# Kernel optimization log

Measured on AMD Instinct MI355X. Metric: run time of the kernel, lower is better.

The kernel has to match this reference:

```python
import jax, jax.numpy as jnp
import numpy as np

B, F0, D = 512, 40, 32
SIZES = [200, 200, 200]


def _glorot(key, shape):
    fan_in, fan_out = shape[0], shape[1]
    std = np.sqrt(2.0 / (fan_in + fan_out)).astype(np.float32)
    return jax.random.normal(key, shape, dtype=jnp.float32) * std


def setup_inputs() -> dict:
    key = jax.random.key(0)
    k0, k1, k2, k3 = jax.random.split(key, 4)
    inputs = jax.random.normal(k0, (B, F0, D), dtype=jnp.float32)
    # weights: (field_i * field_0, next_size), matching tf conv1d filter (1, Fi*F0, next)
    W0 = _glorot(k1, (F0 * F0, SIZES[0]))
    W1 = _glorot(k2, (SIZES[0] * F0, SIZES[1]))
    W2 = _glorot(k3, (SIZES[1] * F0, SIZES[2]))
    return {"inputs": inputs, "W0": W0, "W1": W1, "W2": W2}


def _cin(inputs, Ws):
    # inputs: [B, F0, D]; each layer: outer product along field dims per embedding dim,
    # then a 1x1 'conv' (GEMM) mixing the F0*Fi interaction axis down to next size.
    h = inputs
    outs = []
    for W in Ws:
        # z[b,i,j,d] = x0[b,i,d] * h[b,j,d]  -> flatten (i,j) row-major (matches tf reshape)
        z = jnp.einsum('bid,bjd->bijd', inputs, h)
        b, f0, fi, d = z.shape
        z = z.reshape(b, f0 * fi, d)
        # conv1d with kernel width 1 == GEMM over the interaction axis
        h = jnp.einsum('bkd,kn->bnd', z, W)  # [B, next, D]
        outs.append(h)
    out = jnp.concatenate(outs, axis=1)      # [B, sum(sizes), D]
    return jnp.sum(out, axis=-1)             # [B, sum(sizes)]


def reference(inputs, W0, W1, W2):
    return _cin(inputs, [W0, W1, W2])
```

## Files before the change

kernel.cpp:

```cpp
#include <hip/hip_runtime.h>

#define CIN_B 512
#define CIN_F0 40
#define CIN_D 32
#define CIN_S 200

typedef _Float16 f16x8 __attribute__((ext_vector_type(8)));
typedef _Float16 f16x2 __attribute__((ext_vector_type(2)));
typedef float floatx16 __attribute__((ext_vector_type(16)));

__device__ __forceinline__ unsigned short f2h(float f) {
    _Float16 h = (_Float16)f;
    return *(unsigned short*)&h;
}
__device__ __forceinline__ float h2f(unsigned short u) {
    return (float)(*(_Float16*)&u);
}
__device__ __forceinline__ f16x8 mulbc(f16x8 v, unsigned int s2) {
    union { unsigned int u; f16x2 p; } sc; sc.u = s2;
    union { f16x8 h; f16x2 p[4]; } a, r;
    a.h = v;
#pragma unroll
    for (int q = 0; q < 4; ++q) r.p[q] = a.p[q] * sc.p;
    return r.h;
}

__global__ __launch_bounds__(256) void prep_all(
    const float* __restrict__ X,  const float* __restrict__ W0,
    const float* __restrict__ W1, const float* __restrict__ W2,
    unsigned short* __restrict__ Wtk1, unsigned short* __restrict__ Wtk2,
    unsigned short* __restrict__ W2t,  unsigned short* __restrict__ X0hd,
    unsigned short* __restrict__ Xh) {
    __shared__ unsigned short T[32][33];
    const int bid = blockIdx.x;

    if (bid < 120) {
        const int kc = bid, nn = threadIdx.x;
        const int i = kc / 3, kk = kc - i * 3;
        unsigned short v[16];
#pragma unroll
        for (int kw = 0; kw < 16; ++kw) {
            int j = kk * 16 + kw;
            float f = 0.f;
            if (j < CIN_F0 && nn < CIN_S) f = W0[(size_t)(i * CIN_F0 + j) * CIN_S + nn];
            v[kw] = f2h(f);
        }
        uint4* dst = (uint4*)(Wtk1 + ((size_t)kc * 256 + nn) * 16);
        dst[0] = ((const uint4*)v)[0];
        dst[1] = ((const uint4*)v)[1];
    } else if (bid < 640) {
        const int kc = bid - 120, nn = threadIdx.x;
        const int i = kc / 13, kk = kc - i * 13;
        const float sc = (kk == 6) ? 0.5f : 1.0f;
        unsigned short v[16];
#pragma unroll
        for (int kw = 0; kw < 16; ++kw) {
            int j = kk * 16 + kw;
            float f = 0.f;
            if (j < CIN_S && nn < CIN_S) f = sc * W1[(size_t)(i * CIN_S + j) * CIN_S + nn];
            v[kw] = f2h(f);
        }
        uint4* dst = (uint4*)(Wtk2 + ((size_t)kc * 256 + nn) * 16);
        dst[0] = ((const uint4*)v)[0];
        dst[1] = ((const uint4*)v)[1];
    } else if (bid < 2432) {
        const int q0 = bid - 640;
        const int kt = q0 & 255, nt = q0 >> 8;
        const int tx = threadIdx.x & 31, ty = threadIdx.x >> 5;
#pragma unroll
        for (int q = 0; q < 4; ++q) {
            int kl = ty + 8 * q;
            int k = kt * 32 + kl, n = nt * 32 + tx;
            float f = (k < 8000 && n < CIN_S) ? W2[(size_t)k * CIN_S + n] : 0.f;
            T[kl][tx] = f2h(f);
        }
        __syncthreads();
#pragma unroll
        for (int q = 0; q < 4; ++q) {
            int nl = ty + 8 * q;
            W2t[(size_t)(nt * 32 + nl) * 8192 + kt * 32 + tx] = T[tx][nl];
        }
    } else {
        int e = (bid - 2432) * 256 + threadIdx.x;
        int d = e & 31;
        int rest = e >> 5;
        int i = rest % CIN_F0;
        int b = rest / CIN_F0;
        unsigned short v = f2h(X[e]);
        Xh[e] = v;
        X0hd[((size_t)b * CIN_D + d) * 48 + i] = v;
        if (e < CIN_B * CIN_D * 8) {
            int q = e & 7, dd = (e >> 3) & 31, bb = e >> 8;
            X0hd[((size_t)bb * CIN_D + dd) * 48 + 40 + q] = 0;
        }
    }
}

template <int NKC, int KCPI_TOT, int JROW, int MODE, int NB, int WPS>
__global__ __launch_bounds__(448, WPS)
void cin_layer(const unsigned short* __restrict__ Hsrc,
               const unsigned short* __restrict__ Xh,
               const unsigned short* __restrict__ Wtk,
               unsigned short* __restrict__ Hout,
               float* __restrict__ outp) {
    __shared__ __align__(16) unsigned short Bp[NB * NKC * 512];
    __shared__ unsigned int Xl[CIN_F0 * CIN_D];

    const int tid = threadIdx.x;
    const int b0 = blockIdx.x * NB;
    const int jh = (MODE == 1) ? 0 : blockIdx.y;
    const int kks = jh * 6;

    for (int e = tid; e < CIN_F0 * CIN_D; e += 448) {
        unsigned int lo = Xh[(size_t)b0 * (CIN_F0 * CIN_D) + e];
        unsigned int hi = (NB == 2) ? (unsigned int)Xh[(size_t)(b0 + 1) * (CIN_F0 * CIN_D) + e] : 0u;
        Xl[e] = lo | (hi << 16);
    }
    {
        const int j0 = (MODE == 1) ? 0 : jh * 96;
        uint4* Bpu = (uint4*)Bp;
        for (int g = tid; g < NB * 64 * NKC; g += 448) {
            int bb = g / (64 * NKC), r = g - bb * (64 * NKC);
            int d = r / (2 * NKC), c = r - d * (2 * NKC);
            uint4 v = ((const uint4*)Hsrc)[(((size_t)(b0 + bb) * CIN_D + d) * JROW + j0) / 8 + c];
            Bpu[(bb * NKC + (c >> 1)) * 64 + (c & 1) * 32 + d] = v;
        }
    }
    __syncthreads();

    const int wave = tid >> 6, lane = tid & 63;
    const int l32 = lane & 31, hl = lane >> 5;
    const int tile = wave;

    const int aB = (tile * 32 + l32) * 16 + hl * 8;
    constexpr int NS = 20 * NKC;

    f16x8 Ar[2][2];
    f16x8 Br[2][NB];

    auto ldA = [&](int s, int slot) {
        int ss = (s < NS) ? s : (NS - 1);
        int iA = 2 * (ss / NKC), kk = ss % NKC;
        int e = (iA * KCPI_TOT + kks + kk) * 4096 + aB;
        Ar[slot][0] = *(const f16x8*)(Wtk + e);
        Ar[slot][1] = *(const f16x8*)(Wtk + e + KCPI_TOT * 4096);
    };
    auto ldB = [&](int s, int slot) {
        int ss = (s < NS) ? s : (NS - 1);
        int kk = ss % NKC;
        Br[slot][0] = *(const f16x8*)&Bp[(0 * NKC + kk) * 512 + lane * 8];
        if constexpr (NB == 2)
            Br[slot][1] = *(const f16x8*)&Bp[(1 * NKC + kk) * 512 + lane * 8];
    };

    ldA(0, 0);
    ldA(1, 1);
    ldB(0, 0);

    floatx16 acc0, acc1;
#pragma unroll
    for (int r = 0; r < 16; ++r) acc0[r] = 0.f;
    if constexpr (NB == 2) {
#pragma unroll
        for (int r = 0; r < 16; ++r) acc1[r] = 0.f;
    }
    unsigned int xs0a = 0, xs1a = 0, xs0b = 0, xs1b = 0;

#pragma unroll 1
    for (int s0 = 0; s0 < NS; s0 += 2 * NKC) {
#pragma unroll
        for (int t = 0; t < 2 * NKC; ++t) {
            const int s = s0 + t;
            const int kk = t % NKC;
            if (kk == 0) {
                const int iA = (s0 / NKC + (t ? 1 : 0)) * 2;
                unsigned int xpa = Xl[iA * CIN_D + l32];
                unsigned int xpb = Xl[(iA + 1) * CIN_D + l32];
                xs0a = (xpa & 0xffffu) | (xpa << 16);
                xs0b = (xpb & 0xffffu) | (xpb << 16);
                if constexpr (NB == 2) {
                    xs1a = (xpa >> 16) | (xpa & 0xffff0000u);
                    xs1b = (xpb >> 16) | (xpb & 0xffff0000u);
                }
            }
            ldB(s + 1, (t + 1) & 1);
            const int sl = t & 1;
            acc0 = __builtin_amdgcn_mfma_f32_32x32x16_f16(
                Ar[sl][0], mulbc(Br[sl][0], xs0a), acc0, 0, 0, 0);
            if constexpr (NB == 2)
                acc1 = __builtin_amdgcn_mfma_f32_32x32x16_f16(
                    Ar[sl][0], mulbc(Br[sl][1], xs1a), acc1, 0, 0, 0);
            acc0 = __builtin_amdgcn_mfma_f32_32x32x16_f16(
                Ar[sl][1], mulbc(Br[sl][0], xs0b), acc0, 0, 0, 0);
            if constexpr (NB == 2)
                acc1 = __builtin_amdgcn_mfma_f32_32x32x16_f16(
                    Ar[sl][1], mulbc(Br[sl][1], xs1b), acc1, 0, 0, 0);
            ldA(s + 2, sl);
        }
    }

#pragma unroll
    for (int bb = 0; bb < NB; ++bb) {
        const floatx16& a = bb ? acc1 : acc0;

        if constexpr (MODE == 1) {
            unsigned short* dst =
                Hout + ((size_t)(b0 + bb) * CIN_D + l32) * 224 + tile * 32;
#pragma unroll
            for (int qd = 0; qd < 4; ++qd) {
                ushort4 pk;
                pk.x = f2h(a[4 * qd + 0]);
                pk.y = f2h(a[4 * qd + 1]);
                pk.z = f2h(a[4 * qd + 2]);
                pk.w = f2h(a[4 * qd + 3]);
                *(ushort4*)&dst[8 * qd + 4 * hl] = pk;
            }
        }
        if constexpr (MODE == 2) {
            unsigned short* hb2 =
                Hout + (((size_t)jh * CIN_B + b0 + bb) * 208) * CIN_D + l32;
#pragma unroll
            for (int r = 0; r < 16; ++r) {
                int n = tile * 32 + (r & 3) + 8 * (r >> 2) + 4 * hl;
                if (n < 208) hb2[(size_t)n * CIN_D] = f2h(a[r]);
            }
        }

#pragma unroll
        for (int r = 0; r < 16; ++r) {
            float v = a[r];
            v += __shfl_xor(v, 1);
            v += __shfl_xor(v, 2);
            v += __shfl_xor(v, 4);
            v += __shfl_xor(v, 8);
            v += __shfl_xor(v, 16);
            if (l32 == 0) {
                int n = tile * 32 + (r & 3) + 8 * (r >> 2) + 4 * hl;
                if (n < CIN_S) {
                    if constexpr (MODE == 1)
                        outp[(size_t)(b0 + bb) * 600 + n] = v;
                    else
                        outp[((size_t)jh * CIN_B + b0 + bb) * CIN_S + n] = v;
                }
            }
        }
    }
}

__global__ __launch_bounds__(448) void cin_g(const unsigned short* __restrict__ Xh,
                                             const unsigned short* __restrict__ Hacc,
                                             unsigned short* __restrict__ G) {
    const int b = blockIdx.x;
    const int wave = threadIdx.x >> 6, lane = threadIdx.x & 63;
    const int l32 = lane & 31, hl = lane >> 5;
    const int jt = wave;

    if (wave == 0 && lane < 24) {
        uint4 z; z.x = z.y = z.z = z.w = 0;
        ((uint4*)(G + (size_t)b * 8192 + 8000))[lane] = z;
    }

    f16x8 zed;
#pragma unroll
    for (int q = 0; q < 8; ++q) zed[q] = (_Float16)0.f;

    f16x8 a[2][2];
#pragma unroll
    for (int it = 0; it < 2; ++it) {
        int i = it * 32 + l32;
#pragma unroll
        for (int kh = 0; kh < 2; ++kh)
            a[it][kh] = (i < CIN_F0)
                ? *(const f16x8*)&Xh[((size_t)b * CIN_F0 + i) * CIN_D + kh * 16 + hl * 8]
                : zed;
    }

    const int j = jt * 32 + l32;
    const unsigned short* p0 = Hacc + ((size_t)b * 208 + j) * CIN_D;
    const unsigned short* p1 = Hacc + ((size_t)(CIN_B + b) * 208 + j) * CIN_D;
    f16x8 bf[2];
#pragma unroll
    for (int kh = 0; kh < 2; ++kh)
        bf[kh] = (j < 208)
            ? (*(const f16x8*)(p0 + kh * 16 + hl * 8) +
               *(const f16x8*)(p1 + kh * 16 + hl * 8))
            : zed;

#pragma unroll
    for (int it = 0; it < 2; ++it) {
        floatx16 acc;
#pragma unroll
        for (int r = 0; r < 16; ++r) acc[r] = 0.f;
        acc = __builtin_amdgcn_mfma_f32_32x32x16_f16(a[it][0], bf[0], acc, 0, 0, 0);
        acc = __builtin_amdgcn_mfma_f32_32x32x16_f16(a[it][1], bf[1], acc, 0, 0, 0);
#pragma unroll
        for (int r = 0; r < 16; ++r) {
            int row = (r & 3) + 8 * (r >> 2) + 4 * hl;
            int i = it * 32 + row, jj = jt * 32 + l32;
            if (i < CIN_F0 && jj < CIN_S)
                G[(size_t)b * 8192 + i * CIN_S + jj] = f2h(acc[r]);
        }
    }
}

__global__ __launch_bounds__(64) void cin_l3(const unsigned short* __restrict__ W2t,
                                             const unsigned short* __restrict__ G,
                                             float* __restrict__ outp3) {
    const int mt = blockIdx.x;
    const int bt = blockIdx.y;
    const int kch = blockIdx.z;
    const int lane = threadIdx.x, l32 = lane & 31, hl = lane >> 5;

    const unsigned short* pa = W2t + (size_t)(mt * 32 + l32) * 8192 + kch * 512 + hl * 8;
    const unsigned short* pb = G   + (size_t)(bt * 32 + l32) * 8192 + kch * 512 + hl * 8;

    floatx16 acc;
#pragma unroll
    for (int r = 0; r < 16; ++r) acc[r] = 0.f;

    f16x8 Aa[2], Bb[2];
    Aa[0] = *(const f16x8*)(pa);       Bb[0] = *(const f16x8*)(pb);
    Aa[1] = *(const f16x8*)(pa + 16);  Bb[1] = *(const f16x8*)(pb + 16);

#pragma unroll 1
    for (int s0 = 0; s0 < 32; s0 += 2) {
#pragma unroll
        for (int t = 0; t < 2; ++t) {
            acc = __builtin_amdgcn_mfma_f32_32x32x16_f16(Aa[t], Bb[t], acc, 0, 0, 0);
            Aa[t] = *(const f16x8*)(pa + (s0 + t + 2) * 16);
            Bb[t] = *(const f16x8*)(pb + (s0 + t + 2) * 16);
        }
    }

#pragma unroll
    for (int r = 0; r < 16; ++r) {
        int n = mt * 32 + (r & 3) + 8 * (r >> 2) + 4 * hl;
        if (n < CIN_S)
            outp3[((size_t)kch * CIN_B + bt * 32 + l32) * CIN_S + n] = acc[r];
    }
}

__global__ __launch_bounds__(256) void cin_outc(const float* __restrict__ p2,
                                                const float* __restrict__ p3,
                                                float* __restrict__ out) {
    int e = blockIdx.x * 256 + threadIdx.x;
    int b = e / 400, t = e - b * 400;
    int half = t / 200, n = t - half * 200;
    float s;
    if (half == 0) {
        s = p2[(size_t)b * CIN_S + n] + p2[(size_t)(CIN_B + b) * CIN_S + n];
    } else {
        s = 0.f;
#pragma unroll
        for (int q = 0; q < 16; ++q)
            s += p3[((size_t)q * CIN_B + b) * CIN_S + n];
    }
    out[(size_t)b * 600 + 200 + half * 200 + n] = s;
}

extern "C" void kernel_launch(void* const* d_in, const int* in_sizes, int n_in,
                              void* d_out, int out_size, void* d_ws, size_t ws_size,
                              hipStream_t stream) {
    const float* X  = (const float*)d_in[0];
    const float* W0 = (const float*)d_in[1];
    const float* W1 = (const float*)d_in[2];
    const float* W2 = (const float*)d_in[3];
    float* out = (float*)d_out;

    unsigned short* Wtk1 = (unsigned short*)d_ws;
    unsigned short* Wtk2 = Wtk1 + (size_t)120 * 4096;
    unsigned short* W2t  = Wtk2 + (size_t)520 * 4096;
    unsigned short* X0hd = W2t + (size_t)224 * 8192;
    unsigned short* Xh   = X0hd + (size_t)CIN_B * CIN_D * 48;
    unsigned short* H1   = Xh + (size_t)CIN_B * CIN_F0 * CIN_D;
    unsigned short* Hacc = H1 + (size_t)CIN_B * CIN_D * 224;
    float* outp2 = (float*)(Hacc + (size_t)2 * CIN_B * 208 * CIN_D);
    float* outp3 = outp2 + (size_t)2 * CIN_B * CIN_S;
    unsigned short* G = (unsigned short*)(outp3 + (size_t)16 * CIN_B * CIN_S);

    prep_all<<<4992, 256, 0, stream>>>(X, W0, W1, W2, Wtk1, Wtk2, W2t, X0hd, Xh);

    cin_layer<3, 3, 48, 1, 2, 4><<<dim3(CIN_B / 2, 1), 448, 0, stream>>>(
        X0hd, Xh, Wtk1, H1, out);
    cin_layer<7, 13, 224, 2, 2, 4><<<dim3(CIN_B / 2, 2), 448, 0, stream>>>(
        H1, Xh, Wtk2, Hacc, outp2);

    cin_g<<<CIN_B, 448, 0, stream>>>(Xh, Hacc, G);
    cin_l3<<<dim3(7, 16, 16), 64, 0, stream>>>(W2t, G, outp3);

    cin_outc<<<(CIN_B * 400) / 256, 256, 0, stream>>>(outp2, outp3, out);
}
```

Measured before the change: 209.5 us.

## Split layer-1 interaction axis across two blocks with partial-sum reduction

Layer 1 now runs over a 2D grid that splits the i (field) reduction into two halves. Each half writes a partial fp16 H1 buffer and partial row sums. Layer 2 adds the two partial H1 buffers when it loads its B tiles, and the final combine kernel also reduces the layer-1 partial sums. The aim is to double the block count of the small first layer for better occupancy and latency hiding. The cost is extra partial-buffer traffic, an fp16 rounding of the partials before summation, and G now aliasing the H1 buffer.

```diff
diff --git a/kernel.cpp b/kernel.cpp
--- a/kernel.cpp
+++ b/kernel.cpp
@@ -96,33 +96,42 @@
     }
 }
 
-template <int NKC, int KCPI_TOT, int JROW, int MODE, int NB, int WPS>
-__global__ __launch_bounds__(448, WPS)
+template <int NKC, int KCPI_TOT, int JROW, int MODE, int IH, bool HSUM>
+__global__ __launch_bounds__(448, 4)
 void cin_layer(const unsigned short* __restrict__ Hsrc,
                const unsigned short* __restrict__ Xh,
                const unsigned short* __restrict__ Wtk,
                unsigned short* __restrict__ Hout,
                float* __restrict__ outp) {
-    __shared__ __align__(16) unsigned short Bp[NB * NKC * 512];
+    __shared__ __align__(16) unsigned short Bp[2 * NKC * 512];
     __shared__ unsigned int Xl[CIN_F0 * CIN_D];
 
     const int tid = threadIdx.x;
-    const int b0 = blockIdx.x * NB;
+    const int b0 = blockIdx.x * 2;
     const int jh = (MODE == 1) ? 0 : blockIdx.y;
+    const int ih = (MODE == 1 && IH == 2) ? blockIdx.y : 0;
     const int kks = jh * 6;
+    constexpr int IBASE_STEP = CIN_F0 / IH;
 
     for (int e = tid; e < CIN_F0 * CIN_D; e += 448) {
         unsigned int lo = Xh[(size_t)b0 * (CIN_F0 * CIN_D) + e];
-        unsigned int hi = (NB == 2) ? (unsigned int)Xh[(size_t)(b0 + 1) * (CIN_F0 * CIN_D) + e] : 0u;
+        unsigned int hi = Xh[(size_t)(b0 + 1) * (CIN_F0 * CIN_D) + e];
         Xl[e] = lo | (hi << 16);
     }
     {
         const int j0 = (MODE == 1) ? 0 : jh * 96;
+        constexpr size_t HPART = (size_t)CIN_B * CIN_D * 224;
         uint4* Bpu = (uint4*)Bp;
-        for (int g = tid; g < NB * 64 * NKC; g += 448) {
+        for (int g = tid; g < 2 * 64 * NKC; g += 448) {
             int bb = g / (64 * NKC), r = g - bb * (64 * NKC);
             int d = r / (2 * NKC), c = r - d * (2 * NKC);
-            uint4 v = ((const uint4*)Hsrc)[(((size_t)(b0 + bb) * CIN_D + d) * JROW + j0) / 8 + c];
+            size_t idx = (((size_t)(b0 + bb) * CIN_D + d) * JROW + j0) / 8 + c;
+            uint4 v = ((const uint4*)Hsrc)[idx];
+            if constexpr (HSUM) {
+                uint4 v1 = ((const uint4*)(Hsrc + HPART))[idx];
+                f16x8 s = *(f16x8*)&v + *(f16x8*)&v1;
+                v = *(uint4*)&s;
+            }
             Bpu[(bb * NKC + (c >> 1)) * 64 + (c & 1) * 32 + d] = v;
         }
     }
@@ -134,23 +143,27 @@
 
     const int aB = (tile * 32 + l32) * 16 + hl * 8;
     constexpr int NS = 20 * NKC;
+    constexpr int NSI = NS / IH;
+
+    const unsigned short* WtkB =
+        Wtk + (size_t)(ih * IBASE_STEP) * KCPI_TOT * 4096;
+    const unsigned int* XlB = Xl + ih * IBASE_STEP * CIN_D;
 
     f16x8 Ar[2][2];
-    f16x8 Br[2][NB];
+    f16x8 Br[2][2];
 
     auto ldA = [&](int s, int slot) {
-        int ss = (s < NS) ? s : (NS - 1);
+        int ss = (s < NSI) ? s : (NSI - 1);
         int iA = 2 * (ss / NKC), kk = ss % NKC;
-        int e = (iA * KCPI_TOT + kks + kk) * 4096 + aB;
-        Ar[slot][0] = *(const f16x8*)(Wtk + e);
-        Ar[slot][1] = *(const f16x8*)(Wtk + e + KCPI_TOT * 4096);
+        size_t e = (size_t)(iA * KCPI_TOT + kks + kk) * 4096 + aB;
+        Ar[slot][0] = *(const f16x8*)(WtkB + e);
+        Ar[slot][1] = *(const f16x8*)(WtkB + e + (size_t)KCPI_TOT * 4096);
     };
     auto ldB = [&](int s, int slot) {
-        int ss = (s < NS) ? s : (NS - 1);
+        int ss = (s < NSI) ? s : (NSI - 1);
         int kk = ss % NKC;
         Br[slot][0] = *(const f16x8*)&Bp[(0 * NKC + kk) * 512 + lane * 8];
-        if constexpr (NB == 2)
-            Br[slot][1] = *(const f16x8*)&Bp[(1 * NKC + kk) * 512 + lane * 8];
+        Br[slot][1] = *(const f16x8*)&Bp[(1 * NKC + kk) * 512 + lane * 8];
     };
 
     ldA(0, 0);
@@ -159,53 +172,46 @@
 
     floatx16 acc0, acc1;
 #pragma unroll
-    for (int r = 0; r < 16; ++r) acc0[r] = 0.f;
-    if constexpr (NB == 2) {
-#pragma unroll
-        for (int r = 0; r < 16; ++r) acc1[r] = 0.f;
-    }
+    for (int r = 0; r < 16; ++r) { acc0[r] = 0.f; acc1[r] = 0.f; }
     unsigned int xs0a = 0, xs1a = 0, xs0b = 0, xs1b = 0;
 
 #pragma unroll 1
-    for (int s0 = 0; s0 < NS; s0 += 2 * NKC) {
+    for (int s0 = 0; s0 < NSI; s0 += 2 * NKC) {
 #pragma unroll
         for (int t = 0; t < 2 * NKC; ++t) {
             const int s = s0 + t;
             const int kk = t % NKC;
             if (kk == 0) {
                 const int iA = (s0 / NKC + (t ? 1 : 0)) * 2;
-                unsigned int xpa = Xl[iA * CIN_D + l32];
-                unsigned int xpb = Xl[(iA + 1) * CIN_D + l32];
+                unsigned int xpa = XlB[iA * CIN_D + l32];
+                unsigned int xpb = XlB[(iA + 1) * CIN_D + l32];
                 xs0a = (xpa & 0xffffu) | (xpa << 16);
+                xs1a = (xpa >> 16) | (xpa & 0xffff0000u);
                 xs0b = (xpb & 0xffffu) | (xpb << 16);
-                if constexpr (NB == 2) {
-                    xs1a = (xpa >> 16) | (xpa & 0xffff0000u);
-                    xs1b = (xpb >> 16) | (xpb & 0xffff0000u);
-                }
+                xs1b = (xpb >> 16) | (xpb & 0xffff0000u);
             }
             ldB(s + 1, (t + 1) & 1);
             const int sl = t & 1;
             acc0 = __builtin_amdgcn_mfma_f32_32x32x16_f16(
                 Ar[sl][0], mulbc(Br[sl][0], xs0a), acc0, 0, 0, 0);
-            if constexpr (NB == 2)
-                acc1 = __builtin_amdgcn_mfma_f32_32x32x16_f16(
-                    Ar[sl][0], mulbc(Br[sl][1], xs1a), acc1, 0, 0, 0);
+            acc1 = __builtin_amdgcn_mfma_f32_32x32x16_f16(
+                Ar[sl][0], mulbc(Br[sl][1], xs1a), acc1, 0, 0, 0);
             acc0 = __builtin_amdgcn_mfma_f32_32x32x16_f16(
                 Ar[sl][1], mulbc(Br[sl][0], xs0b), acc0, 0, 0, 0);
-            if constexpr (NB == 2)
-                acc1 = __builtin_amdgcn_mfma_f32_32x32x16_f16(
-                    Ar[sl][1], mulbc(Br[sl][1], xs1b), acc1, 0, 0, 0);
+            acc1 = __builtin_amdgcn_mfma_f32_32x32x16_f16(
+                Ar[sl][1], mulbc(Br[sl][1], xs1b), acc1, 0, 0, 0);
             ldA(s + 2, sl);
         }
     }
 
 #pragma unroll
-    for (int bb = 0; bb < NB; ++bb) {
+    for (int bb = 0; bb < 2; ++bb) {
         const floatx16& a = bb ? acc1 : acc0;
 
         if constexpr (MODE == 1) {
             unsigned short* dst =
-                Hout + ((size_t)(b0 + bb) * CIN_D + l32) * 224 + tile * 32;
+                Hout + (size_t)ih * CIN_B * CIN_D * 224 +
+                ((size_t)(b0 + bb) * CIN_D + l32) * 224 + tile * 32;
 #pragma unroll
             for (int qd = 0; qd < 4; ++qd) {
                 ushort4 pk;
@@ -226,6 +232,7 @@
             }
         }
 
+        const int part = (MODE == 1) ? ih : jh;
 #pragma unroll
         for (int r = 0; r < 16; ++r) {
             float v = a[r];
@@ -236,12 +243,8 @@
             v += __shfl_xor(v, 16);
             if (l32 == 0) {
                 int n = tile * 32 + (r & 3) + 8 * (r >> 2) + 4 * hl;
-                if (n < CIN_S) {
-                    if constexpr (MODE == 1)
-                        outp[(size_t)(b0 + bb) * 600 + n] = v;
-                    else
-                        outp[((size_t)jh * CIN_B + b0 + bb) * CIN_S + n] = v;
-                }
+                if (n < CIN_S)
+                    outp[((size_t)part * CIN_B + b0 + bb) * CIN_S + n] = v;
             }
         }
     }
@@ -340,14 +343,17 @@
     }
 }
 
-__global__ __launch_bounds__(256) void cin_outc(const float* __restrict__ p2,
+__global__ __launch_bounds__(256) void cin_outc(const float* __restrict__ p1,
+                                                const float* __restrict__ p2,
                                                 const float* __restrict__ p3,
                                                 float* __restrict__ out) {
     int e = blockIdx.x * 256 + threadIdx.x;
-    int b = e / 400, t = e - b * 400;
-    int half = t / 200, n = t - half * 200;
+    int b = e / 600, t = e - b * 600;
+    int sec = t / 200, n = t - sec * 200;
     float s;
-    if (half == 0) {
+    if (sec == 0) {
+        s = p1[(size_t)b * CIN_S + n] + p1[(size_t)(CIN_B + b) * CIN_S + n];
+    } else if (sec == 1) {
         s = p2[(size_t)b * CIN_S + n] + p2[(size_t)(CIN_B + b) * CIN_S + n];
     } else {
         s = 0.f;
@@ -355,7 +361,7 @@
         for (int q = 0; q < 16; ++q)
             s += p3[((size_t)q * CIN_B + b) * CIN_S + n];
     }
-    out[(size_t)b * 600 + 200 + half * 200 + n] = s;
+    out[e] = s;
 }
 
 extern "C" void kernel_launch(void* const* d_in, const int* in_sizes, int n_in,
@@ -372,21 +378,22 @@
     unsigned short* W2t  = Wtk2 + (size_t)520 * 4096;
     unsigned short* X0hd = W2t + (size_t)224 * 8192;
     unsigned short* Xh   = X0hd + (size_t)CIN_B * CIN_D * 48;
-    unsigned short* H1   = Xh + (size_t)CIN_B * CIN_F0 * CIN_D;
-    unsigned short* Hacc = H1 + (size_t)CIN_B * CIN_D * 224;
-    float* outp2 = (float*)(Hacc + (size_t)2 * CIN_B * 208 * CIN_D);
+    unsigned short* H1p  = Xh + (size_t)CIN_B * CIN_F0 * CIN_D;
+    unsigned short* Hacc = H1p + (size_t)2 * CIN_B * CIN_D * 224;
+    float* outp1 = (float*)(Hacc + (size_t)2 * CIN_B * 208 * CIN_D);
+    float* outp2 = outp1 + (size_t)2 * CIN_B * CIN_S;
     float* outp3 = outp2 + (size_t)2 * CIN_B * CIN_S;
-    unsigned short* G = (unsigned short*)(outp3 + (size_t)16 * CIN_B * CIN_S);
+    unsigned short* G = H1p;
 
     prep_all<<<4992, 256, 0, stream>>>(X, W0, W1, W2, Wtk1, Wtk2, W2t, X0hd, Xh);
 
-    cin_layer<3, 3, 48, 1, 2, 4><<<dim3(CIN_B / 2, 1), 448, 0, stream>>>(
-        X0hd, Xh, Wtk1, H1, out);
-    cin_layer<7, 13, 224, 2, 2, 4><<<dim3(CIN_B / 2, 2), 448, 0, stream>>>(
-        H1, Xh, Wtk2, Hacc, outp2);
+    cin_layer<3, 3, 48, 1, 2, false><<<dim3(CIN_B / 2, 2), 448, 0, stream>>>(
+        X0hd, Xh, Wtk1, H1p, outp1);
+    cin_layer<7, 13, 224, 2, 1, true><<<dim3(CIN_B / 2, 2), 448, 0, stream>>>(
+        H1p, Xh, Wtk2, Hacc, outp2);
 
     cin_g<<<CIN_B, 448, 0, stream>>>(Xh, Hacc, G);
     cin_l3<<<dim3(7, 16, 16), 64, 0, stream>>>(W2t, G, outp3);
 
-    cin_outc<<<(CIN_B * 400) / 256, 256, 0, stream>>>(outp2, outp3, out);
-}
+    cin_outc<<<(CIN_B * 600) / 256, 256, 0, stream>>>(outp1, outp2, outp3, out);
+}
```

Result: no change. 212.6 us (+1.5%).

## Stage layer-2 weights through an LDS ring via async global-to-LDS loads

Applied to the files above, without the earlier changes.

Layer 2 now runs as a 896-thread block covering four batch rows. The block's two wave groups share weight tiles that are streamed into a 4-slot LDS ring with global_load_lds, paced by vmcnt waits and barriers. Before, each wave loaded A fragments straight from global memory per step. The goal is to cut redundant global weight traffic and overlap weight fetches with MFMA work, at the cost of a barrier per step and larger LDS use, which may lower occupancy. Layer 1 is split into its own specialised kernel.

```diff
diff --git a/kernel.cpp b/kernel.cpp
--- a/kernel.cpp
+++ b/kernel.cpp
@@ -23,6 +23,11 @@
 #pragma unroll
     for (int q = 0; q < 4; ++q) r.p[q] = a.p[q] * sc.p;
     return r.h;
+}
+__device__ __forceinline__ void gload_lds16(const unsigned short* g, unsigned short* l) {
+    __builtin_amdgcn_global_load_lds(
+        (const __attribute__((address_space(1))) void*)(const void*)g,
+        (__attribute__((address_space(3))) void*)(void*)l, 16, 0, 0);
 }
 
 __global__ __launch_bounds__(256) void prep_all(
@@ -96,33 +101,30 @@
     }
 }
 
-template <int NKC, int KCPI_TOT, int JROW, int MODE, int NB, int WPS>
-__global__ __launch_bounds__(448, WPS)
-void cin_layer(const unsigned short* __restrict__ Hsrc,
-               const unsigned short* __restrict__ Xh,
-               const unsigned short* __restrict__ Wtk,
-               unsigned short* __restrict__ Hout,
-               float* __restrict__ outp) {
-    __shared__ __align__(16) unsigned short Bp[NB * NKC * 512];
+template <int NKC, int KCPI_TOT, int JROW>
+__global__ __launch_bounds__(448, 4)
+void cin_layer1(const unsigned short* __restrict__ Hsrc,
+                const unsigned short* __restrict__ Xh,
+                const unsigned short* __restrict__ Wtk,
+                unsigned short* __restrict__ Hout,
+                float* __restrict__ outp) {
+    __shared__ __align__(16) unsigned short Bp[2 * NKC * 512];
     __shared__ unsigned int Xl[CIN_F0 * CIN_D];
 
     const int tid = threadIdx.x;
-    const int b0 = blockIdx.x * NB;
-    const int jh = (MODE == 1) ? 0 : blockIdx.y;
-    const int kks = jh * 6;
+    const int b0 = blockIdx.x * 2;
 
     for (int e = tid; e < CIN_F0 * CIN_D; e += 448) {
         unsigned int lo = Xh[(size_t)b0 * (CIN_F0 * CIN_D) + e];
-        unsigned int hi = (NB == 2) ? (unsigned int)Xh[(size_t)(b0 + 1) * (CIN_F0 * CIN_D) + e] : 0u;
+        unsigned int hi = Xh[(size_t)(b0 + 1) * (CIN_F0 * CIN_D) + e];
         Xl[e] = lo | (hi << 16);
     }
     {
-        const int j0 = (MODE == 1) ? 0 : jh * 96;
         uint4* Bpu = (uint4*)Bp;
-        for (int g = tid; g < NB * 64 * NKC; g += 448) {
+        for (int g = tid; g < 2 * 64 * NKC; g += 448) {
             int bb = g / (64 * NKC), r = g - bb * (64 * NKC);
             int d = r / (2 * NKC), c = r - d * (2 * NKC);
-            uint4 v = ((const uint4*)Hsrc)[(((size_t)(b0 + bb) * CIN_D + d) * JROW + j0) / 8 + c];
+            uint4 v = ((const uint4*)Hsrc)[(((size_t)(b0 + bb) * CIN_D + d) * JROW) / 8 + c];
             Bpu[(bb * NKC + (c >> 1)) * 64 + (c & 1) * 32 + d] = v;
         }
     }
@@ -136,12 +138,12 @@
     constexpr int NS = 20 * NKC;
 
     f16x8 Ar[2][2];
-    f16x8 Br[2][NB];
+    f16x8 Br[2][2];
 
     auto ldA = [&](int s, int slot) {
         int ss = (s < NS) ? s : (NS - 1);
         int iA = 2 * (ss / NKC), kk = ss % NKC;
-        int e = (iA * KCPI_TOT + kks + kk) * 4096 + aB;
+        int e = (iA * KCPI_TOT + kk) * 4096 + aB;
         Ar[slot][0] = *(const f16x8*)(Wtk + e);
         Ar[slot][1] = *(const f16x8*)(Wtk + e + KCPI_TOT * 4096);
     };
@@ -149,8 +151,7 @@
         int ss = (s < NS) ? s : (NS - 1);
         int kk = ss % NKC;
         Br[slot][0] = *(const f16x8*)&Bp[(0 * NKC + kk) * 512 + lane * 8];
-        if constexpr (NB == 2)
-            Br[slot][1] = *(const f16x8*)&Bp[(1 * NKC + kk) * 512 + lane * 8];
+        Br[slot][1] = *(const f16x8*)&Bp[(1 * NKC + kk) * 512 + lane * 8];
     };
 
     ldA(0, 0);
@@ -159,11 +160,7 @@
 
     floatx16 acc0, acc1;
 #pragma unroll
-    for (int r = 0; r < 16; ++r) acc0[r] = 0.f;
-    if constexpr (NB == 2) {
-#pragma unroll
-        for (int r = 0; r < 16; ++r) acc1[r] = 0.f;
-    }
+    for (int r = 0; r < 16; ++r) { acc0[r] = 0.f; acc1[r] = 0.f; }
     unsigned int xs0a = 0, xs1a = 0, xs0b = 0, xs1b = 0;
 
 #pragma unroll 1
@@ -177,55 +174,38 @@
                 unsigned int xpa = Xl[iA * CIN_D + l32];
                 unsigned int xpb = Xl[(iA + 1) * CIN_D + l32];
                 xs0a = (xpa & 0xffffu) | (xpa << 16);
+                xs1a = (xpa >> 16) | (xpa & 0xffff0000u);
                 xs0b = (xpb & 0xffffu) | (xpb << 16);
-                if constexpr (NB == 2) {
-                    xs1a = (xpa >> 16) | (xpa & 0xffff0000u);
-                    xs1b = (xpb >> 16) | (xpb & 0xffff0000u);
-                }
+                xs1b = (xpb >> 16) | (xpb & 0xffff0000u);
             }
             ldB(s + 1, (t + 1) & 1);
             const int sl = t & 1;
             acc0 = __builtin_amdgcn_mfma_f32_32x32x16_f16(
                 Ar[sl][0], mulbc(Br[sl][0], xs0a), acc0, 0, 0, 0);
-            if constexpr (NB == 2)
-                acc1 = __builtin_amdgcn_mfma_f32_32x32x16_f16(
-                    Ar[sl][0], mulbc(Br[sl][1], xs1a), acc1, 0, 0, 0);
+            acc1 = __builtin_amdgcn_mfma_f32_32x32x16_f16(
+                Ar[sl][0], mulbc(Br[sl][1], xs1a), acc1, 0, 0, 0);
             acc0 = __builtin_amdgcn_mfma_f32_32x32x16_f16(
                 Ar[sl][1], mulbc(Br[sl][0], xs0b), acc0, 0, 0, 0);
-            if constexpr (NB == 2)
-                acc1 = __builtin_amdgcn_mfma_f32_32x32x16_f16(
-                    Ar[sl][1], mulbc(Br[sl][1], xs1b), acc1, 0, 0, 0);
+            acc1 = __builtin_amdgcn_mfma_f32_32x32x16_f16(
+                Ar[sl][1], mulbc(Br[sl][1], xs1b), acc1, 0, 0, 0);
             ldA(s + 2, sl);
         }
     }
 
 #pragma unroll
-    for (int bb = 0; bb < NB; ++bb) {
+    for (int bb = 0; bb < 2; ++bb) {
         const floatx16& a = bb ? acc1 : acc0;
-
-        if constexpr (MODE == 1) {
-            unsigned short* dst =
-                Hout + ((size_t)(b0 + bb) * CIN_D + l32) * 224 + tile * 32;
-#pragma unroll
-            for (int qd = 0; qd < 4; ++qd) {
-                ushort4 pk;
-                pk.x = f2h(a[4 * qd + 0]);
-                pk.y = f2h(a[4 * qd + 1]);
-                pk.z = f2h(a[4 * qd + 2]);
-                pk.w = f2h(a[4 * qd + 3]);
-                *(ushort4*)&dst[8 * qd + 4 * hl] = pk;
-            }
-        }
-        if constexpr (MODE == 2) {
-            unsigned short* hb2 =
-                Hout + (((size_t)jh * CIN_B + b0 + bb) * 208) * CIN_D + l32;
-#pragma unroll
-            for (int r = 0; r < 16; ++r) {
-                int n = tile * 32 + (r & 3) + 8 * (r >> 2) + 4 * hl;
-                if (n < 208) hb2[(size_t)n * CIN_D] = f2h(a[r]);
-            }
-        }
-
+        unsigned short* dst =
+            Hout + ((size_t)(b0 + bb) * CIN_D + l32) * 224 + tile * 32;
+#pragma unroll
+        for (int qd = 0; qd < 4; ++qd) {
+            ushort4 pk;
+            pk.x = f2h(a[4 * qd + 0]);
+            pk.y = f2h(a[4 * qd + 1]);
+            pk.z = f2h(a[4 * qd + 2]);
+            pk.w = f2h(a[4 * qd + 3]);
+            *(ushort4*)&dst[8 * qd + 4 * hl] = pk;
+        }
 #pragma unroll
         for (int r = 0; r < 16; ++r) {
             float v = a[r];
@@ -236,12 +216,133 @@
             v += __shfl_xor(v, 16);
             if (l32 == 0) {
                 int n = tile * 32 + (r & 3) + 8 * (r >> 2) + 4 * hl;
-                if (n < CIN_S) {
-                    if constexpr (MODE == 1)
-                        outp[(size_t)(b0 + bb) * 600 + n] = v;
-                    else
-                        outp[((size_t)jh * CIN_B + b0 + bb) * CIN_S + n] = v;
-                }
+                if (n < CIN_S) outp[(size_t)(b0 + bb) * 600 + n] = v;
+            }
+        }
+    }
+}
+
+template <int NKC, int KCPI_TOT, int JROW>
+__global__ __launch_bounds__(896, 4)
+void cin_l2s(const unsigned short* __restrict__ Hsrc,
+             const unsigned short* __restrict__ Xh,
+             const unsigned short* __restrict__ Wtk,
+             unsigned short* __restrict__ Hout,
+             float* __restrict__ outp) {
+    __shared__ __align__(16) unsigned short Bp[4 * NKC * 512];
+    __shared__ unsigned int Xl[2][CIN_F0 * CIN_D];
+    __shared__ __align__(16) unsigned short Ring[4 * 7 * 512 * 2];
+
+    const int tid = threadIdx.x;
+    const int b0 = blockIdx.x * 4;
+    const int jh = blockIdx.y;
+    const int kks = jh * 6;
+    constexpr int NS = 20 * NKC;
+
+    for (int e = tid; e < 2 * CIN_F0 * CIN_D; e += 896) {
+        int pair = e / (CIN_F0 * CIN_D), ee = e - pair * (CIN_F0 * CIN_D);
+        unsigned int lo = Xh[(size_t)(b0 + 2 * pair) * (CIN_F0 * CIN_D) + ee];
+        unsigned int hi = Xh[(size_t)(b0 + 2 * pair + 1) * (CIN_F0 * CIN_D) + ee];
+        Xl[pair][ee] = lo | (hi << 16);
+    }
+    {
+        const int j0 = jh * 96;
+        uint4* Bpu = (uint4*)Bp;
+        for (int g = tid; g < 4 * 64 * NKC; g += 896) {
+            int bb = g / (64 * NKC), r = g - bb * (64 * NKC);
+            int d = r / (2 * NKC), c = r - d * (2 * NKC);
+            uint4 v = ((const uint4*)Hsrc)[(((size_t)(b0 + bb) * CIN_D + d) * JROW + j0) / 8 + c];
+            Bpu[(bb * NKC + (c >> 1)) * 64 + (c & 1) * 32 + d] = v;
+        }
+    }
+
+    const int wave = tid >> 6, lane = tid & 63;
+    const int l32 = lane & 31, hl = lane >> 5;
+    const int wg = wave / 7;
+    const int nt = wave - wg * 7;
+    constexpr int SLOT = 7 * 512 * 2;
+
+    const unsigned short* gS =
+        Wtk + (size_t)(kks + wg * KCPI_TOT) * 4096 + (size_t)(nt * 64 + lane) * 8;
+    const int destB = wg * 3584 + nt * 512;
+
+#pragma unroll
+    for (int s = 0; s < 3; ++s) {
+        gload_lds16(gS, Ring + s * SLOT + destB);
+        gS += 4096;
+    }
+    __syncthreads();
+
+    const unsigned short* BpW = Bp + (size_t)(2 * wg) * NKC * 512 + lane * 8;
+    const unsigned short* ringR = Ring + l32 * 16 + hl * 8 + nt * 512;
+    const unsigned int* XlW = Xl[wg] + l32;
+
+    floatx16 acc0, acc1;
+#pragma unroll
+    for (int r = 0; r < 16; ++r) { acc0[r] = 0.f; acc1[r] = 0.f; }
+    unsigned int xs0a = 0, xs1a = 0, xs0b = 0, xs1b = 0;
+
+#pragma unroll 1
+    for (int s0 = 0; s0 < NS; s0 += 2 * NKC) {
+#pragma unroll
+        for (int t = 0; t < 2 * NKC; ++t) {
+            const int kk = t % NKC;
+            asm volatile("s_waitcnt vmcnt(2)" ::: "memory");
+            asm volatile("s_barrier" ::: "memory");
+            gload_lds16(gS, Ring + ((s0 + t + 3) & 3) * SLOT + destB);
+            {
+                const int kk3 = (t + 3) % NKC;
+                gS += (kk3 == NKC - 1) ? (size_t)(2 * KCPI_TOT - (NKC - 1)) * 4096
+                                       : (size_t)4096;
+            }
+            if (kk == 0) {
+                const int iA = (s0 / NKC + (t ? 1 : 0)) * 2;
+                unsigned int xpa = XlW[iA * CIN_D];
+                unsigned int xpb = XlW[(iA + 1) * CIN_D];
+                xs0a = (xpa & 0xffffu) | (xpa << 16);
+                xs1a = (xpa >> 16) | (xpa & 0xffff0000u);
+                xs0b = (xpb & 0xffffu) | (xpb << 16);
+                xs1b = (xpb >> 16) | (xpb & 0xffff0000u);
+            }
+            const unsigned short* sp = ringR + ((s0 + t) & 3) * SLOT;
+            f16x8 A0 = *(const f16x8*)(sp);
+            f16x8 A1 = *(const f16x8*)(sp + 3584);
+            f16x8 b0f = *(const f16x8*)(BpW + (0 * NKC + kk) * 512);
+            f16x8 b1f = *(const f16x8*)(BpW + (1 * NKC + kk) * 512);
+            acc0 = __builtin_amdgcn_mfma_f32_32x32x16_f16(
+                A0, mulbc(b0f, xs0a), acc0, 0, 0, 0);
+            acc1 = __builtin_amdgcn_mfma_f32_32x32x16_f16(
+                A0, mulbc(b1f, xs1a), acc1, 0, 0, 0);
+            acc0 = __builtin_amdgcn_mfma_f32_32x32x16_f16(
+                A1, mulbc(b0f, xs0b), acc0, 0, 0, 0);
+            acc1 = __builtin_amdgcn_mfma_f32_32x32x16_f16(
+                A1, mulbc(b1f, xs1b), acc1, 0, 0, 0);
+        }
+    }
+
+#pragma unroll
+    for (int bb = 0; bb < 2; ++bb) {
+        const floatx16& a = bb ? acc1 : acc0;
+        const int b = b0 + 2 * wg + bb;
+        unsigned short* hb2 =
+            Hout + (((size_t)jh * CIN_B + b) * 208) * CIN_D + l32;
+#pragma unroll
+        for (int r = 0; r < 16; ++r) {
+            int n = nt * 32 + (r & 3) + 8 * (r >> 2) + 4 * hl;
+            if (n < 208) hb2[(size_t)n * CIN_D] = f2h(a[r]);
+        }
+#pragma unroll
+        for (int r = 0; r < 16; ++r) {
+            float v = a[r];
+            v += __shfl_xor(v, 1);
+            v += __shfl_xor(v, 2);
+            v += __shfl_xor(v, 4);
+            v += __shfl_xor(v, 8);
+            v += __shfl_xor(v, 16);
+            if (l32 == 0) {
+                int n = nt * 32 + (r & 3) + 8 * (r >> 2) + 4 * hl;
+                if (n < CIN_S)
+                    outp[((size_t)jh * CIN_B + b) * CIN_S + n] = v;
             }
         }
     }
@@ -380,9 +481,9 @@
 
     prep_all<<<4992, 256, 0, stream>>>(X, W0, W1, W2, Wtk1, Wtk2, W2t, X0hd, Xh);
 
-    cin_layer<3, 3, 48, 1, 2, 4><<<dim3(CIN_B / 2, 1), 448, 0, stream>>>(
+    cin_layer1<3, 3, 48><<<dim3(CIN_B / 2, 1), 448, 0, stream>>>(
         X0hd, Xh, Wtk1, H1, out);
-    cin_layer<7, 13, 224, 2, 2, 4><<<dim3(CIN_B / 2, 2), 448, 0, stream>>>(
+    cin_l2s<7, 13, 224><<<dim3(CIN_B / 4, 2), 896, 0, stream>>>(
         H1, Xh, Wtk2, Hacc, outp2);
 
     cin_g<<<CIN_B, 448, 0, stream>>>(Xh, Hacc, G);
```

Result: no change. 209.3 us (-0.1%).
